# Kernel tuning notes

Hardware: AMD Instinct MI355X
Metric: run time of the kernel (lower is better)

Reference implementation:

```python
import jax, jax.numpy as jnp
import numpy as np

B, N, C = 2, 2048, 1024
H, D = 16, 64
EPS = 1e-12  # F.normalize eps


def l2norm(t):
    # torch F.normalize: t / max(||t||_2, eps)
    n = jnp.sqrt(jnp.sum(t * t, axis=-1, keepdims=True))
    return t / jnp.maximum(n, EPS)


def setup_inputs() -> dict:
    key = jax.random.key(0)
    ks = jax.random.split(key, 4)
    x = jax.random.normal(ks[0], (B, N, C), dtype=jnp.float32)
    W_qkv = jax.random.normal(ks[1], (C, 3 * H * D), dtype=jnp.float32) * (1.0 / np.sqrt(C))
    W_out = jax.random.normal(ks[2], (H * D, C), dtype=jnp.float32) * (1.0 / np.sqrt(H * D))
    pos_bias = jax.random.normal(ks[3], (H, N, N), dtype=jnp.float32) * 0.1
    temperature = jnp.array(15.5, dtype=jnp.float32)
    mask = jnp.zeros((B, N), dtype=bool)  # True = padded token
    return {"x": x, "W_qkv": W_qkv, "W_out": W_out, "temperature": temperature,
            "pos_bias": pos_bias, "mask": mask}


def reference(x, W_qkv, W_out, temperature, pos_bias, mask):
    b, n, c = x.shape
    # qkv projection; torch rearrange 'b n (h d qkv) -> qkv b h n d'
    qkv = (x @ W_qkv).reshape(b, n, H, D, 3)
    q = jnp.transpose(qkv[..., 0], (0, 2, 1, 3))  # b h n d
    k = jnp.transpose(qkv[..., 1], (0, 2, 1, 3))
    v = jnp.transpose(qkv[..., 2], (0, 2, 1, 3))
    q, k = l2norm(q), l2norm(k)
    dots = jnp.einsum('bhid,bhjd->bhij', q, k) * temperature
    dots = dots + pos_bias[None]  # broadcast over batch
    qkmask = ~mask  # True = valid
    allowed = qkmask[:, None, :, None] & qkmask[:, None, None, :]
    neg = -jnp.finfo(dots.dtype).max
    dots = jnp.where(allowed, dots, neg)
    attn = jax.nn.softmax(dots, axis=-1)
    out = jnp.einsum('bhij,bhjd->bhid', attn, v)
    out = jnp.transpose(out, (0, 2, 1, 3)).reshape(b, n, H * D)
    return out @ W_out
```

## Files before the change

kernel.cpp:

```cpp
#include <hip/hip_runtime.h>


using short4v = __attribute__((ext_vector_type(4))) short;
using short8 = __attribute__((ext_vector_type(8))) short;
using bf16x8 = __attribute__((ext_vector_type(8))) __bf16;
using f32x4  = __attribute__((ext_vector_type(4))) float;
using int4v  = __attribute__((ext_vector_type(4))) int;

constexpr int Bb = 2, Nn = 2048, Cc = 1024, Hh = 16, Dd = 64;

__device__ __forceinline__ unsigned short f2b(float f) {
  unsigned int u = __float_as_uint(f);
  u += 0x7FFFu + ((u >> 16) & 1u);
  return (unsigned short)(u >> 16);
}
__device__ __forceinline__ float b2f(unsigned short h) {
  return __uint_as_float(((unsigned int)h) << 16);
}
__device__ __forceinline__ f32x4 MFMA(short8 a, short8 b, f32x4 c) {
  return __builtin_amdgcn_mfma_f32_16x16x32_bf16(
      __builtin_bit_cast(bf16x8, a), __builtin_bit_cast(bf16x8, b), c, 0, 0, 0);
}
__device__ __forceinline__ unsigned cvtpk(float lo, float hi) {
  unsigned r;
  asm("v_cvt_pk_bf16_f32 %0, %1, %2" : "=v"(r) : "v"(lo), "v"(hi));
  return r;
}

__global__ void split_plain(const float* __restrict__ in, unsigned short* __restrict__ hi,
                            unsigned short* __restrict__ lo, int n) {
  int i = blockIdx.x * 256 + threadIdx.x;
  if (i < n) {
    float v = in[i];
    unsigned short t = f2b(v);
    hi[i] = t; lo[i] = f2b(v - b2f(t));
  }
}

__global__ __launch_bounds__(256) void split_trans2(
    const float* __restrict__ in, unsigned short* __restrict__ hi,
    unsigned short* __restrict__ lo, int K, int N) {
  __shared__ float t[32][33];
  int k0 = blockIdx.y * 32, n0 = blockIdx.x * 32;
  int tx = threadIdx.x & 31, ty = threadIdx.x >> 5;
  #pragma unroll
  for (int i = 0; i < 4; i++)
    t[ty + i * 8][tx] = in[(size_t)(k0 + ty + i * 8) * N + n0 + tx];
  __syncthreads();
  #pragma unroll
  for (int i = 0; i < 4; i++) {
    float v = t[tx][ty + i * 8];
    size_t o = (size_t)(n0 + ty + i * 8) * K + k0 + tx;
    unsigned short h = f2b(v);
    hi[o] = h; lo[o] = f2b(v - b2f(h));
  }
}

__global__ __launch_bounds__(256, 3) void gemm3(
    const unsigned short* __restrict__ Ah, const unsigned short* __restrict__ Al,
    const unsigned short* __restrict__ Bh, const unsigned short* __restrict__ Bl,
    float* __restrict__ C, int M, int N, int K) {
  __shared__ unsigned short sAh[128][40], sAl[128][40], sBh[128][40], sBl[128][40];
  int tid = threadIdx.x;
  int w = tid >> 6, l = tid & 63;
  int wr = w >> 1, wc = w & 1;
  int mrow = l & 15, kg = l >> 4;
  int row0 = blockIdx.y * 128, col0 = blockIdx.x * 128;
  f32x4 z = {0.f, 0.f, 0.f, 0.f};
  f32x4 acc[4][4];
  for (int i = 0; i < 4; i++) for (int j = 0; j < 4; j++) acc[i][j] = z;
  int sr = tid >> 1, sc0 = (tid & 1) * 16;
  for (int k0 = 0; k0 < K; k0 += 32) {
    const unsigned short* pa = Ah + (size_t)(row0 + sr) * K + k0 + sc0;
    const unsigned short* pal = Al + (size_t)(row0 + sr) * K + k0 + sc0;
    const unsigned short* pb = Bh + (size_t)(col0 + sr) * K + k0 + sc0;
    const unsigned short* pbl = Bl + (size_t)(col0 + sr) * K + k0 + sc0;
    short8 tA0 = *(const short8*)pa,  tA1 = *(const short8*)(pa + 8);
    short8 tL0 = *(const short8*)pal, tL1 = *(const short8*)(pal + 8);
    short8 tB0 = *(const short8*)pb,  tB1 = *(const short8*)(pb + 8);
    short8 tC0 = *(const short8*)pbl, tC1 = *(const short8*)(pbl + 8);
    __syncthreads();
    *(short8*)&sAh[sr][sc0] = tA0; *(short8*)&sAh[sr][sc0 + 8] = tA1;
    *(short8*)&sAl[sr][sc0] = tL0; *(short8*)&sAl[sr][sc0 + 8] = tL1;
    *(short8*)&sBh[sr][sc0] = tB0; *(short8*)&sBh[sr][sc0 + 8] = tB1;
    *(short8*)&sBl[sr][sc0] = tC0; *(short8*)&sBl[sr][sc0 + 8] = tC1;
    __syncthreads();
    short8 ah_[4], al_[4], bh_[4], bl_[4];
    #pragma unroll
    for (int mt = 0; mt < 4; mt++) {
      ah_[mt] = *(const short8*)&sAh[wr * 64 + mt * 16 + mrow][kg * 8];
      al_[mt] = *(const short8*)&sAl[wr * 64 + mt * 16 + mrow][kg * 8];
    }
    #pragma unroll
    for (int nt = 0; nt < 4; nt++) {
      bh_[nt] = *(const short8*)&sBh[wc * 64 + nt * 16 + mrow][kg * 8];
      bl_[nt] = *(const short8*)&sBl[wc * 64 + nt * 16 + mrow][kg * 8];
    }
    __builtin_amdgcn_s_setprio(1);
    #pragma unroll
    for (int mt = 0; mt < 4; mt++)
      #pragma unroll
      for (int nt = 0; nt < 4; nt++) {
        acc[mt][nt] = MFMA(ah_[mt], bh_[nt], acc[mt][nt]);
        acc[mt][nt] = MFMA(al_[mt], bh_[nt], acc[mt][nt]);
        acc[mt][nt] = MFMA(ah_[mt], bl_[nt], acc[mt][nt]);
      }
    __builtin_amdgcn_s_setprio(0);
  }
  #pragma unroll
  for (int mt = 0; mt < 4; mt++)
    #pragma unroll
    for (int nt = 0; nt < 4; nt++)
      #pragma unroll
      for (int q = 0; q < 4; q++) {
        int row = row0 + wr * 64 + mt * 16 + kg * 4 + q;
        int col = col0 + wc * 64 + nt * 16 + mrow;
        C[(size_t)row * N + col] = acc[mt][nt][q];
      }
}

__global__ __launch_bounds__(256) void qkv_post2(
    const float* __restrict__ qkv,
    unsigned short* __restrict__ qh, unsigned short* __restrict__ ql,
    unsigned short* __restrict__ kh, unsigned short* __restrict__ kl,
    unsigned short* __restrict__ vth) {
  __shared__ unsigned short vt[64][72];
  int tid = threadIdx.x, w = tid >> 6, d = tid & 63;
  int bid = blockIdx.x;
  int nb = bid & 31, h = (bid >> 5) & 15, b = bid >> 9;
  size_t head = (size_t)(b * Hh + h);
  int n0 = nb * 64;
  for (int it = 0; it < 16; it++) {
    int nl = w * 16 + it;
    int n = n0 + nl;
    const float* src = qkv + (size_t)(b * Nn + n) * 3072 + h * 192 + d * 3;
    float qv = src[0], kv = src[1], vv = src[2];
    float q2 = qv * qv, k2 = kv * kv;
    #pragma unroll
    for (int m = 1; m < 64; m <<= 1) { q2 += __shfl_xor(q2, m); k2 += __shfl_xor(k2, m); }
    qv /= fmaxf(sqrtf(q2), 1e-12f);
    kv /= fmaxf(sqrtf(k2), 1e-12f);
    size_t o = (head * Nn + n) * Dd + d;
    unsigned short tq = f2b(qv); qh[o] = tq; ql[o] = f2b(qv - b2f(tq));
    unsigned short tk = f2b(kv); kh[o] = tk; kl[o] = f2b(kv - b2f(tk));
    vt[nl][d] = f2b(vv);
  }
  __syncthreads();
  int r = tid >> 2, cq = (tid & 3) * 16;
  short8 x0, x1;
  #pragma unroll
  for (int i = 0; i < 8; i++) ((short*)&x0)[i] = (short)vt[cq + i][r];
  #pragma unroll
  for (int i = 0; i < 8; i++) ((short*)&x1)[i] = (short)vt[cq + 8 + i][r];
  unsigned short* dst = vth + (head * Dd + r) * Nn + n0 + cq;
  *(short8*)dst = x0;
  *(short8*)(dst + 8) = x1;
}

__global__ __launch_bounds__(256, 2) void flash_attn5(
    const unsigned short* __restrict__ qh_g, const unsigned short* __restrict__ ql_g,
    const unsigned short* __restrict__ kh_g, const unsigned short* __restrict__ kl_g,
    const unsigned short* __restrict__ vh_g,
    const float* __restrict__ bias, const float* __restrict__ tptr,
    unsigned short* __restrict__ ah, unsigned short* __restrict__ al) {
  __shared__ unsigned short sKh[2][64][64], sKl[2][64][64], sVh[2][64][64];
  int tid = threadIdx.x, w = tid >> 6, l = tid & 63;
  int mrow = l & 15, kg = l >> 4;
  int bid = blockIdx.x;
  int b = bid & 1, h = (bid >> 1) & 15, ib = bid >> 5;
  float T = tptr[0];
  const float L2E = 1.44269504f;
  float Tl2 = T * L2E;
  float negMs = -(T + 1.0f) * L2E;
  size_t head = (size_t)(b * Hh + h);
  int i0 = ib * 128 + w * 32;
  short8 aqh0[2], aql0[2], aqh1[2], aql1[2];
  {
    size_t qb0 = (head * Nn + i0 + mrow) * Dd;
    size_t qb1 = (head * Nn + i0 + 16 + mrow) * Dd;
    #pragma unroll
    for (int kk = 0; kk < 2; kk++) {
      aqh0[kk] = *(const short8*)(qh_g + qb0 + kk * 32 + kg * 8);
      aql0[kk] = *(const short8*)(ql_g + qb0 + kk * 32 + kg * 8);
      aqh1[kk] = *(const short8*)(qh_g + qb1 + kk * 32 + kg * 8);
      aql1[kk] = *(const short8*)(ql_g + qb1 + kk * 32 + kg * 8);
    }
  }
  f32x4 Ot0[4], Ot1[4];
  #pragma unroll
  for (int dt = 0; dt < 4; dt++) { Ot0[dt] = {0.f,0.f,0.f,0.f}; Ot1[dt] = {0.f,0.f,0.f,0.f}; }
  float L0 = 0.f, L1 = 0.f;

  int r0 = tid >> 3, c0 = (tid & 7) * 8;
  int r1 = r0 + 32;
  int lk0 = r0 * 64 + (c0 ^ ((r0 & 7) << 3));
  int lk1 = r1 * 64 + (c0 ^ ((r1 & 7) << 3));
  int pr0 = (r0 & 32) | ((r0 & 12) << 1) | ((r0 & 16) >> 2) | (r0 & 3);
  int pr1 = (r1 & 32) | ((r1 & 12) << 1) | ((r1 & 16) >> 2) | (r1 & 3);
  const unsigned short* kh_b = kh_g + head * Nn * Dd;
  const unsigned short* kl_b = kl_g + head * Nn * Dd;
  const unsigned short* vh_b = vh_g + head * Dd * Nn;
  const float* bbA = bias + ((size_t)h * Nn + i0 + mrow) * Nn + kg * 8;
  const float* bbB = bbA + (size_t)16 * Nn;

  short8 rKh0, rKh1, rKl0, rKl1, rVh0, rVh1;
  f32x4 rB0[4], rB1[4];

  auto issueKV = [&](int j0) {
    rKh0 = *(const short8*)(kh_b + (size_t)(j0 + pr0) * Dd + c0);
    rKh1 = *(const short8*)(kh_b + (size_t)(j0 + pr1) * Dd + c0);
    rKl0 = *(const short8*)(kl_b + (size_t)(j0 + pr0) * Dd + c0);
    rKl1 = *(const short8*)(kl_b + (size_t)(j0 + pr1) * Dd + c0);
    rVh0 = *(const short8*)(vh_b + (size_t)r0 * Nn + j0 + c0);
    rVh1 = *(const short8*)(vh_b + (size_t)r1 * Nn + j0 + c0);
  };
  auto writeKV = [&](int dst) {
    *(short8*)((unsigned short*)sKh[dst] + lk0) = rKh0;
    *(short8*)((unsigned short*)sKh[dst] + lk1) = rKh1;
    *(short8*)((unsigned short*)sKl[dst] + lk0) = rKl0;
    *(short8*)((unsigned short*)sKl[dst] + lk1) = rKl1;
    *(short8*)((unsigned short*)sVh[dst] + lk0) = rVh0;
    *(short8*)((unsigned short*)sVh[dst] + lk1) = rVh1;
  };
  auto issueBias = [&](int j0) {
    rB0[0] = *(const f32x4*)(bbA + j0);
    rB0[1] = *(const f32x4*)(bbA + j0 + 4);
    rB0[2] = *(const f32x4*)(bbA + j0 + 32);
    rB0[3] = *(const f32x4*)(bbA + j0 + 36);
    rB1[0] = *(const f32x4*)(bbB + j0);
    rB1[1] = *(const f32x4*)(bbB + j0 + 4);
    rB1[2] = *(const f32x4*)(bbB + j0 + 32);
    rB1[3] = *(const f32x4*)(bbB + j0 + 36);
    #pragma unroll
    for (int i = 0; i < 4; i++) {
      rB0[i] = rB0[i] * L2E + negMs;
      rB1[i] = rB1[i] * L2E + negMs;
    }
  };
  auto softmax = [&](f32x4* s, f32x4* rB, float& L_, short8& pf0, short8& pf1) {
    float p_[4][4];
    float ps = 0.f;
    #pragma unroll
    for (int jt = 0; jt < 4; jt++)
      #pragma unroll
      for (int q = 0; q < 4; q++) {
        p_[jt][q] = __builtin_amdgcn_exp2f(fmaf(s[jt][q], Tl2, rB[jt][q]));
        ps += p_[jt][q];
      }
    L_ += ps;
    unsigned pk[8];
    #pragma unroll
    for (int jt = 0; jt < 4; jt++) {
      pk[2 * jt]     = cvtpk(p_[jt][0], p_[jt][1]);
      pk[2 * jt + 1] = cvtpk(p_[jt][2], p_[jt][3]);
    }
    int4v w0 = {(int)pk[0], (int)pk[1], (int)pk[2], (int)pk[3]};
    int4v w1 = {(int)pk[4], (int)pk[5], (int)pk[6], (int)pk[7]};
    pf0 = __builtin_bit_cast(short8, w0);
    pf1 = __builtin_bit_cast(short8, w1);
  };

  issueKV(0);
  issueBias(0);
  writeKV(0);
  __syncthreads();
  issueKV(64);

  for (int t = 0; t < 32; t++) {
    int j0 = t * 64;
    int cur = t & 1;
    f32x4 s0[4], s1[4];
    #pragma unroll
    for (int jt = 0; jt < 4; jt++) { s0[jt] = {0.f,0.f,0.f,0.f}; s1[jt] = {0.f,0.f,0.f,0.f}; }
    __builtin_amdgcn_s_setprio(1);
    #pragma unroll
    for (int jt = 0; jt < 4; jt++) {
      int row = jt * 16 + mrow;
      int swz = (row & 7) << 3;
      #pragma unroll
      for (int kk = 0; kk < 2; kk++) {
        short8 bh = *(const short8*)&sKh[cur][row][(kk * 32 + kg * 8) ^ swz];
        short8 bl = *(const short8*)&sKl[cur][row][(kk * 32 + kg * 8) ^ swz];
        s0[jt] = MFMA(bh, aqh0[kk], s0[jt]);
        s0[jt] = MFMA(bh, aql0[kk], s0[jt]);
        s0[jt] = MFMA(bl, aqh0[kk], s0[jt]);
        s1[jt] = MFMA(bh, aqh1[kk], s1[jt]);
        s1[jt] = MFMA(bh, aql1[kk], s1[jt]);
        s1[jt] = MFMA(bl, aqh1[kk], s1[jt]);
      }
    }
    __builtin_amdgcn_s_setprio(0);
    short8 pfA0, pfA1, pfB0, pfB1;
    softmax(s0, rB0, L0, pfA0, pfA1);
    softmax(s1, rB1, L1, pfB0, pfB1);
    if (t < 31) issueBias(j0 + 64);
    if (t < 31) writeKV(cur ^ 1);
    if (t < 30) issueKV(j0 + 128);
    __builtin_amdgcn_s_setprio(1);
    #pragma unroll
    for (int dt = 0; dt < 4; dt++) {
      int row = dt * 16 + mrow;
      int swz = (row & 7) << 3;
      short8 va0 = *(const short8*)&sVh[cur][row][(kg * 8) ^ swz];
      short8 va1 = *(const short8*)&sVh[cur][row][(32 + kg * 8) ^ swz];
      Ot0[dt] = MFMA(va0, pfA0, Ot0[dt]);
      Ot0[dt] = MFMA(va1, pfA1, Ot0[dt]);
      Ot1[dt] = MFMA(va0, pfB0, Ot1[dt]);
      Ot1[dt] = MFMA(va1, pfB1, Ot1[dt]);
    }
    __builtin_amdgcn_s_setprio(0);
    __syncthreads();
  }
  L0 += __shfl_xor(L0, 16); L0 += __shfl_xor(L0, 32);
  L1 += __shfl_xor(L1, 16); L1 += __shfl_xor(L1, 32);
  float inv0 = 1.f / L0, inv1 = 1.f / L1;
  size_t orow0 = ((size_t)(b * Nn + i0 + mrow)) * (Hh * Dd) + h * Dd + kg * 4;
  size_t orow1 = ((size_t)(b * Nn + i0 + 16 + mrow)) * (Hh * Dd) + h * Dd + kg * 4;
  #pragma unroll
  for (int dt = 0; dt < 4; dt++) {
    short4v hi4, lo4;
    #pragma unroll
    for (int r = 0; r < 4; r++) {
      float val = Ot0[dt][r] * inv0;
      unsigned short hv = f2b(val);
      hi4[r] = (short)hv;
      lo4[r] = (short)f2b(val - b2f(hv));
    }
    *(short4v*)(ah + orow0 + dt * 16) = hi4;
    *(short4v*)(al + orow0 + dt * 16) = lo4;
    #pragma unroll
    for (int r = 0; r < 4; r++) {
      float val = Ot1[dt][r] * inv1;
      unsigned short hv = f2b(val);
      hi4[r] = (short)hv;
      lo4[r] = (short)f2b(val - b2f(hv));
    }
    *(short4v*)(ah + orow1 + dt * 16) = hi4;
    *(short4v*)(al + orow1 + dt * 16) = lo4;
  }
}

extern "C" void kernel_launch(void* const* d_in, const int* in_sizes, int n_in,
                              void* d_out, int out_size, void* d_ws, size_t ws_size,
                              hipStream_t stream) {
  const float* x    = (const float*)d_in[0];
  const float* Wqkv = (const float*)d_in[1];
  const float* Wout = (const float*)d_in[2];
  const float* temp = (const float*)d_in[3];
  const float* bias = (const float*)d_in[4];
  float* out = (float*)d_out;

  char* ws = (char*)d_ws;
  size_t off = 0;
  auto alloc = [&](size_t bytes) -> void* {
    void* p = ws + off;
    off += (bytes + 255) & ~(size_t)255;
    return p;
  };
  const size_t MT = (size_t)Bb * Nn;
  float* qkv = (float*)alloc(MT * 3072 * 4);
  unsigned short* xh  = (unsigned short*)alloc(MT * Cc * 2);
  unsigned short* xl  = (unsigned short*)alloc(MT * Cc * 2);
  unsigned short* wqh = (unsigned short*)alloc((size_t)3072 * Cc * 2);
  unsigned short* wql = (unsigned short*)alloc((size_t)3072 * Cc * 2);
  unsigned short* woh = (unsigned short*)alloc((size_t)Cc * Cc * 2);
  unsigned short* wol = (unsigned short*)alloc((size_t)Cc * Cc * 2);
  const size_t HND = (size_t)Bb * Hh * Nn * Dd;
  unsigned short* qh  = (unsigned short*)alloc(HND * 2);
  unsigned short* ql  = (unsigned short*)alloc(HND * 2);
  unsigned short* kh  = (unsigned short*)alloc(HND * 2);
  unsigned short* kl  = (unsigned short*)alloc(HND * 2);
  unsigned short* vth = (unsigned short*)alloc(HND * 2);
  unsigned short* ah  = (unsigned short*)alloc(MT * Cc * 2);
  unsigned short* al  = (unsigned short*)alloc(MT * Cc * 2);
  (void)ws_size; (void)in_sizes; (void)n_in; (void)out_size;

  split_plain<<<dim3((int)(MT * Cc / 256)), dim3(256), 0, stream>>>(x, xh, xl, (int)(MT * Cc));
  split_trans2<<<dim3(3072 / 32, Cc / 32), dim3(256), 0, stream>>>(Wqkv, wqh, wql, Cc, 3072);
  split_trans2<<<dim3(Cc / 32, Cc / 32), dim3(256), 0, stream>>>(Wout, woh, wol, Cc, Cc);

  gemm3<<<dim3(3072 / 128, (int)(MT / 128)), dim3(256), 0, stream>>>(
      xh, xl, wqh, wql, qkv, (int)MT, 3072, Cc);

  qkv_post2<<<dim3(Bb * Hh * (Nn / 64)), dim3(256), 0, stream>>>(
      qkv, qh, ql, kh, kl, vth);

  flash_attn5<<<dim3(Bb * Hh * (Nn / 128)), dim3(256), 0, stream>>>(
      qh, ql, kh, kl, vth, bias, temp, ah, al);

  gemm3<<<dim3(Cc / 128, (int)(MT / 128)), dim3(256), 0, stream>>>(
      ah, al, woh, wol, out, (int)MT, Cc, Cc);
}
```

Baseline: 294.5 us.

## Split attention KV range in two and merge partial results in a separate kernel

The flash attention kernel now handles only half of the key/value sequence per block, which doubles the grid. Each block writes unnormalized fp32 partial outputs and row sums into reused workspace. A new merge kernel adds the two partials, normalizes them, and produces the hi/lo bf16 split. The merge stays exact without a running-max correction because softmax uses a fixed upper-bound shift. The intent is more blocks and better load balance across CUs, at the cost of extra global traffic for the fp32 partials and one more kernel launch.

```diff
diff --git a/kernel.cpp b/kernel.cpp
--- a/kernel.cpp
+++ b/kernel.cpp
@@ -8,6 +8,7 @@
 using int4v  = __attribute__((ext_vector_type(4))) int;
 
 constexpr int Bb = 2, Nn = 2048, Cc = 1024, Hh = 16, Dd = 64;
+constexpr int SPLIT = 2, NSPL = Nn / SPLIT;
 
 __device__ __forceinline__ unsigned short f2b(float f) {
   unsigned int u = __float_as_uint(f);
@@ -157,17 +158,18 @@
   *(short8*)(dst + 8) = x1;
 }
 
-__global__ __launch_bounds__(256, 2) void flash_attn5(
+__global__ __launch_bounds__(256, 2) void flash_attn6(
     const unsigned short* __restrict__ qh_g, const unsigned short* __restrict__ ql_g,
     const unsigned short* __restrict__ kh_g, const unsigned short* __restrict__ kl_g,
     const unsigned short* __restrict__ vh_g,
     const float* __restrict__ bias, const float* __restrict__ tptr,
-    unsigned short* __restrict__ ah, unsigned short* __restrict__ al) {
+    float* __restrict__ Of, float* __restrict__ Lf) {
   __shared__ unsigned short sKh[2][64][64], sKl[2][64][64], sVh[2][64][64];
   int tid = threadIdx.x, w = tid >> 6, l = tid & 63;
   int mrow = l & 15, kg = l >> 4;
   int bid = blockIdx.x;
-  int b = bid & 1, h = (bid >> 1) & 15, ib = bid >> 5;
+  int s = bid & 1, ib = (bid >> 1) & 15, b = (bid >> 5) & 1, h = bid >> 6;
+  int jbase = s * NSPL;
   float T = tptr[0];
   const float L2E = 1.44269504f;
   float Tl2 = T * L2E;
@@ -237,14 +239,14 @@
       rB1[i] = rB1[i] * L2E + negMs;
     }
   };
-  auto softmax = [&](f32x4* s, f32x4* rB, float& L_, short8& pf0, short8& pf1) {
+  auto softmax = [&](f32x4* sx, f32x4* rB, float& L_, short8& pf0, short8& pf1) {
     float p_[4][4];
     float ps = 0.f;
     #pragma unroll
     for (int jt = 0; jt < 4; jt++)
       #pragma unroll
       for (int q = 0; q < 4; q++) {
-        p_[jt][q] = __builtin_amdgcn_exp2f(fmaf(s[jt][q], Tl2, rB[jt][q]));
+        p_[jt][q] = __builtin_amdgcn_exp2f(fmaf(sx[jt][q], Tl2, rB[jt][q]));
         ps += p_[jt][q];
       }
     L_ += ps;
@@ -260,14 +262,14 @@
     pf1 = __builtin_bit_cast(short8, w1);
   };
 
-  issueKV(0);
-  issueBias(0);
+  issueKV(jbase);
+  issueBias(jbase);
   writeKV(0);
   __syncthreads();
-  issueKV(64);
-
-  for (int t = 0; t < 32; t++) {
-    int j0 = t * 64;
+  issueKV(jbase + 64);
+
+  for (int t = 0; t < 16; t++) {
+    int j0 = jbase + t * 64;
     int cur = t & 1;
     f32x4 s0[4], s1[4];
     #pragma unroll
@@ -293,9 +295,9 @@
     short8 pfA0, pfA1, pfB0, pfB1;
     softmax(s0, rB0, L0, pfA0, pfA1);
     softmax(s1, rB1, L1, pfB0, pfB1);
-    if (t < 31) issueBias(j0 + 64);
-    if (t < 31) writeKV(cur ^ 1);
-    if (t < 30) issueKV(j0 + 128);
+    if (t < 15) issueBias(j0 + 64);
+    if (t < 15) writeKV(cur ^ 1);
+    if (t < 14) issueKV(j0 + 128);
     __builtin_amdgcn_s_setprio(1);
     #pragma unroll
     for (int dt = 0; dt < 4; dt++) {
@@ -313,31 +315,45 @@
   }
   L0 += __shfl_xor(L0, 16); L0 += __shfl_xor(L0, 32);
   L1 += __shfl_xor(L1, 16); L1 += __shfl_xor(L1, 32);
-  float inv0 = 1.f / L0, inv1 = 1.f / L1;
-  size_t orow0 = ((size_t)(b * Nn + i0 + mrow)) * (Hh * Dd) + h * Dd + kg * 4;
-  size_t orow1 = ((size_t)(b * Nn + i0 + 16 + mrow)) * (Hh * Dd) + h * Dd + kg * 4;
+  size_t prow0 = ((((size_t)s * Bb + b) * Hh + h) * Nn + i0 + mrow) * Dd + kg * 4;
+  size_t prow1 = prow0 + (size_t)16 * Dd;
   #pragma unroll
   for (int dt = 0; dt < 4; dt++) {
-    short4v hi4, lo4;
-    #pragma unroll
-    for (int r = 0; r < 4; r++) {
-      float val = Ot0[dt][r] * inv0;
-      unsigned short hv = f2b(val);
-      hi4[r] = (short)hv;
-      lo4[r] = (short)f2b(val - b2f(hv));
-    }
-    *(short4v*)(ah + orow0 + dt * 16) = hi4;
-    *(short4v*)(al + orow0 + dt * 16) = lo4;
-    #pragma unroll
-    for (int r = 0; r < 4; r++) {
-      float val = Ot1[dt][r] * inv1;
-      unsigned short hv = f2b(val);
-      hi4[r] = (short)hv;
-      lo4[r] = (short)f2b(val - b2f(hv));
-    }
-    *(short4v*)(ah + orow1 + dt * 16) = hi4;
-    *(short4v*)(al + orow1 + dt * 16) = lo4;
-  }
+    *(f32x4*)(Of + prow0 + dt * 16) = Ot0[dt];
+    *(f32x4*)(Of + prow1 + dt * 16) = Ot1[dt];
+  }
+  if (kg == 0) {
+    size_t lrow = (((size_t)s * Bb + b) * Hh + h) * Nn + i0 + mrow;
+    Lf[lrow] = L0;
+    Lf[lrow + 16] = L1;
+  }
+}
+
+__global__ __launch_bounds__(256) void attn_merge(
+    const float* __restrict__ Of, const float* __restrict__ Lf,
+    unsigned short* __restrict__ ah, unsigned short* __restrict__ al) {
+  int gid = blockIdx.x * 256 + threadIdx.x;
+  int row = gid >> 4;
+  int dq = (gid & 15) << 2;
+  int b = row >> 15, h = (row >> 11) & 15, i = row & 2047;
+  const size_t PS = (size_t)Bb * Hh * Nn * Dd;
+  const size_t LS = (size_t)Bb * Hh * Nn;
+  size_t base = ((size_t)(b * Hh + h) * Nn + i) * Dd + dq;
+  f32x4 o0 = *(const f32x4*)(Of + base);
+  f32x4 o1 = *(const f32x4*)(Of + PS + base);
+  size_t lb = (size_t)(b * Hh + h) * Nn + i;
+  float inv = 1.f / (Lf[lb] + Lf[LS + lb]);
+  short4v hi4, lo4;
+  #pragma unroll
+  for (int r = 0; r < 4; r++) {
+    float val = (o0[r] + o1[r]) * inv;
+    unsigned short hv = f2b(val);
+    hi4[r] = (short)hv;
+    lo4[r] = (short)f2b(val - b2f(hv));
+  }
+  size_t o = ((size_t)(b * Nn + i)) * (Hh * Dd) + h * Dd + dq;
+  *(short4v*)(ah + o) = hi4;
+  *(short4v*)(al + o) = lo4;
 }
 
 extern "C" void kernel_launch(void* const* d_in, const int* in_sizes, int n_in,
@@ -373,6 +389,8 @@
   unsigned short* vth = (unsigned short*)alloc(HND * 2);
   unsigned short* ah  = (unsigned short*)alloc(MT * Cc * 2);
   unsigned short* al  = (unsigned short*)alloc(MT * Cc * 2);
+  float* Of = qkv;
+  float* Lf = (float*)wqh;
   (void)ws_size; (void)in_sizes; (void)n_in; (void)out_size;
 
   split_plain<<<dim3((int)(MT * Cc / 256)), dim3(256), 0, stream>>>(x, xh, xl, (int)(MT * Cc));
@@ -385,8 +403,11 @@
   qkv_post2<<<dim3(Bb * Hh * (Nn / 64)), dim3(256), 0, stream>>>(
       qkv, qh, ql, kh, kl, vth);
 
-  flash_attn5<<<dim3(Bb * Hh * (Nn / 128)), dim3(256), 0, stream>>>(
-      qh, ql, kh, kl, vth, bias, temp, ah, al);
+  flash_attn6<<<dim3(Bb * Hh * (Nn / 128) * SPLIT), dim3(256), 0, stream>>>(
+      qh, ql, kh, kl, vth, bias, temp, Of, Lf);
+
+  attn_merge<<<dim3((int)(Bb * Hh * Nn * (Dd / 4) / 256)), dim3(256), 0, stream>>>(
+      Of, Lf, ah, al);
 
   gemm3<<<dim3(Cc / 128, (int)(MT / 128)), dim3(256), 0, stream>>>(
       ah, al, woh, wol, out, (int)MT, Cc, Cc);
```

After: 294.5 us. Within noise of the previous version (+0.0%).

## Load K and V fragments directly from global memory, dropping LDS staging

Applied to the files above, without the earlier changes.

The flash attention kernel stops staging K-high, K-low and V tiles in double-buffered shared memory. Each wave now loads its MFMA operand fragments straight from global memory (through L2 and L1) every iteration, and the per-iteration block barrier is removed. This cuts LDS traffic, shared-memory footprint and synchronisation. In exchange, the four waves in a block each fetch the same K/V data separately, so global and cache traffic rises, and there is no explicit prefetch to hide load latency.

```diff
diff --git a/kernel.cpp b/kernel.cpp
--- a/kernel.cpp
+++ b/kernel.cpp
@@ -157,13 +157,12 @@
   *(short8*)(dst + 8) = x1;
 }
 
-__global__ __launch_bounds__(256, 2) void flash_attn5(
+__global__ __launch_bounds__(256, 2) void flash_attn7(
     const unsigned short* __restrict__ qh_g, const unsigned short* __restrict__ ql_g,
     const unsigned short* __restrict__ kh_g, const unsigned short* __restrict__ kl_g,
     const unsigned short* __restrict__ vh_g,
     const float* __restrict__ bias, const float* __restrict__ tptr,
     unsigned short* __restrict__ ah, unsigned short* __restrict__ al) {
-  __shared__ unsigned short sKh[2][64][64], sKl[2][64][64], sVh[2][64][64];
   int tid = threadIdx.x, w = tid >> 6, l = tid & 63;
   int mrow = l & 15, kg = l >> 4;
   int bid = blockIdx.x;
@@ -191,37 +190,25 @@
   for (int dt = 0; dt < 4; dt++) { Ot0[dt] = {0.f,0.f,0.f,0.f}; Ot1[dt] = {0.f,0.f,0.f,0.f}; }
   float L0 = 0.f, L1 = 0.f;
 
-  int r0 = tid >> 3, c0 = (tid & 7) * 8;
-  int r1 = r0 + 32;
-  int lk0 = r0 * 64 + (c0 ^ ((r0 & 7) << 3));
-  int lk1 = r1 * 64 + (c0 ^ ((r1 & 7) << 3));
-  int pr0 = (r0 & 32) | ((r0 & 12) << 1) | ((r0 & 16) >> 2) | (r0 & 3);
-  int pr1 = (r1 & 32) | ((r1 & 12) << 1) | ((r1 & 16) >> 2) | (r1 & 3);
+  const unsigned short* kAh[4];
+  const unsigned short* kAl[4];
   const unsigned short* kh_b = kh_g + head * Nn * Dd;
   const unsigned short* kl_b = kl_g + head * Nn * Dd;
+  #pragma unroll
+  for (int jt = 0; jt < 4; jt++) {
+    int prow = ((jt & 2) << 4) | ((mrow & 12) << 1) | ((jt & 1) << 2) | (mrow & 3);
+    kAh[jt] = kh_b + (size_t)prow * Dd + kg * 8;
+    kAl[jt] = kl_b + (size_t)prow * Dd + kg * 8;
+  }
+  const unsigned short* vA[4];
   const unsigned short* vh_b = vh_g + head * Dd * Nn;
+  #pragma unroll
+  for (int dt = 0; dt < 4; dt++)
+    vA[dt] = vh_b + (size_t)(dt * 16 + mrow) * Nn + kg * 8;
   const float* bbA = bias + ((size_t)h * Nn + i0 + mrow) * Nn + kg * 8;
   const float* bbB = bbA + (size_t)16 * Nn;
 
-  short8 rKh0, rKh1, rKl0, rKl1, rVh0, rVh1;
   f32x4 rB0[4], rB1[4];
-
-  auto issueKV = [&](int j0) {
-    rKh0 = *(const short8*)(kh_b + (size_t)(j0 + pr0) * Dd + c0);
-    rKh1 = *(const short8*)(kh_b + (size_t)(j0 + pr1) * Dd + c0);
-    rKl0 = *(const short8*)(kl_b + (size_t)(j0 + pr0) * Dd + c0);
-    rKl1 = *(const short8*)(kl_b + (size_t)(j0 + pr1) * Dd + c0);
-    rVh0 = *(const short8*)(vh_b + (size_t)r0 * Nn + j0 + c0);
-    rVh1 = *(const short8*)(vh_b + (size_t)r1 * Nn + j0 + c0);
-  };
-  auto writeKV = [&](int dst) {
-    *(short8*)((unsigned short*)sKh[dst] + lk0) = rKh0;
-    *(short8*)((unsigned short*)sKh[dst] + lk1) = rKh1;
-    *(short8*)((unsigned short*)sKl[dst] + lk0) = rKl0;
-    *(short8*)((unsigned short*)sKl[dst] + lk1) = rKl1;
-    *(short8*)((unsigned short*)sVh[dst] + lk0) = rVh0;
-    *(short8*)((unsigned short*)sVh[dst] + lk1) = rVh1;
-  };
   auto issueBias = [&](int j0) {
     rB0[0] = *(const f32x4*)(bbA + j0);
     rB0[1] = *(const f32x4*)(bbA + j0 + 4);
@@ -237,14 +224,14 @@
       rB1[i] = rB1[i] * L2E + negMs;
     }
   };
-  auto softmax = [&](f32x4* s, f32x4* rB, float& L_, short8& pf0, short8& pf1) {
+  auto softmax = [&](f32x4* sx, f32x4* rB, float& L_, short8& pf0, short8& pf1) {
     float p_[4][4];
     float ps = 0.f;
     #pragma unroll
     for (int jt = 0; jt < 4; jt++)
       #pragma unroll
       for (int q = 0; q < 4; q++) {
-        p_[jt][q] = __builtin_amdgcn_exp2f(fmaf(s[jt][q], Tl2, rB[jt][q]));
+        p_[jt][q] = __builtin_amdgcn_exp2f(fmaf(sx[jt][q], Tl2, rB[jt][q]));
         ps += p_[jt][q];
       }
     L_ += ps;
@@ -260,56 +247,53 @@
     pf1 = __builtin_bit_cast(short8, w1);
   };
 
-  issueKV(0);
   issueBias(0);
-  writeKV(0);
-  __syncthreads();
-  issueKV(64);
 
   for (int t = 0; t < 32; t++) {
     int j0 = t * 64;
-    int cur = t & 1;
+    short8 bh_[4][2], bl_[4][2];
+    #pragma unroll
+    for (int jt = 0; jt < 4; jt++)
+      #pragma unroll
+      for (int kk = 0; kk < 2; kk++) {
+        bh_[jt][kk] = *(const short8*)(kAh[jt] + (size_t)j0 * Dd + kk * 32);
+        bl_[jt][kk] = *(const short8*)(kAl[jt] + (size_t)j0 * Dd + kk * 32);
+      }
     f32x4 s0[4], s1[4];
     #pragma unroll
     for (int jt = 0; jt < 4; jt++) { s0[jt] = {0.f,0.f,0.f,0.f}; s1[jt] = {0.f,0.f,0.f,0.f}; }
     __builtin_amdgcn_s_setprio(1);
     #pragma unroll
-    for (int jt = 0; jt < 4; jt++) {
-      int row = jt * 16 + mrow;
-      int swz = (row & 7) << 3;
+    for (int jt = 0; jt < 4; jt++)
       #pragma unroll
       for (int kk = 0; kk < 2; kk++) {
-        short8 bh = *(const short8*)&sKh[cur][row][(kk * 32 + kg * 8) ^ swz];
-        short8 bl = *(const short8*)&sKl[cur][row][(kk * 32 + kg * 8) ^ swz];
-        s0[jt] = MFMA(bh, aqh0[kk], s0[jt]);
-        s0[jt] = MFMA(bh, aql0[kk], s0[jt]);
-        s0[jt] = MFMA(bl, aqh0[kk], s0[jt]);
-        s1[jt] = MFMA(bh, aqh1[kk], s1[jt]);
-        s1[jt] = MFMA(bh, aql1[kk], s1[jt]);
-        s1[jt] = MFMA(bl, aqh1[kk], s1[jt]);
-      }
-    }
+        s0[jt] = MFMA(bh_[jt][kk], aqh0[kk], s0[jt]);
+        s0[jt] = MFMA(bh_[jt][kk], aql0[kk], s0[jt]);
+        s0[jt] = MFMA(bl_[jt][kk], aqh0[kk], s0[jt]);
+        s1[jt] = MFMA(bh_[jt][kk], aqh1[kk], s1[jt]);
+        s1[jt] = MFMA(bh_[jt][kk], aql1[kk], s1[jt]);
+        s1[jt] = MFMA(bl_[jt][kk], aqh1[kk], s1[jt]);
+      }
     __builtin_amdgcn_s_setprio(0);
+    short8 va_[4][2];
+    #pragma unroll
+    for (int dt = 0; dt < 4; dt++)
+      #pragma unroll
+      for (int k2 = 0; k2 < 2; k2++)
+        va_[dt][k2] = *(const short8*)(vA[dt] + j0 + k2 * 32);
     short8 pfA0, pfA1, pfB0, pfB1;
     softmax(s0, rB0, L0, pfA0, pfA1);
     softmax(s1, rB1, L1, pfB0, pfB1);
     if (t < 31) issueBias(j0 + 64);
-    if (t < 31) writeKV(cur ^ 1);
-    if (t < 30) issueKV(j0 + 128);
     __builtin_amdgcn_s_setprio(1);
     #pragma unroll
     for (int dt = 0; dt < 4; dt++) {
-      int row = dt * 16 + mrow;
-      int swz = (row & 7) << 3;
-      short8 va0 = *(const short8*)&sVh[cur][row][(kg * 8) ^ swz];
-      short8 va1 = *(const short8*)&sVh[cur][row][(32 + kg * 8) ^ swz];
-      Ot0[dt] = MFMA(va0, pfA0, Ot0[dt]);
-      Ot0[dt] = MFMA(va1, pfA1, Ot0[dt]);
-      Ot1[dt] = MFMA(va0, pfB0, Ot1[dt]);
-      Ot1[dt] = MFMA(va1, pfB1, Ot1[dt]);
+      Ot0[dt] = MFMA(va_[dt][0], pfA0, Ot0[dt]);
+      Ot0[dt] = MFMA(va_[dt][1], pfA1, Ot0[dt]);
+      Ot1[dt] = MFMA(va_[dt][0], pfB0, Ot1[dt]);
+      Ot1[dt] = MFMA(va_[dt][1], pfB1, Ot1[dt]);
     }
     __builtin_amdgcn_s_setprio(0);
-    __syncthreads();
   }
   L0 += __shfl_xor(L0, 16); L0 += __shfl_xor(L0, 32);
   L1 += __shfl_xor(L1, 16); L1 += __shfl_xor(L1, 32);
@@ -385,7 +369,7 @@
   qkv_post2<<<dim3(Bb * Hh * (Nn / 64)), dim3(256), 0, stream>>>(
       qkv, qh, ql, kh, kl, vth);
 
-  flash_attn5<<<dim3(Bb * Hh * (Nn / 128)), dim3(256), 0, stream>>>(
+  flash_attn7<<<dim3(Bb * Hh * (Nn / 128)), dim3(256), 0, stream>>>(
       qh, ql, kh, kl, vth, bias, temp, ah, al);
 
   gemm3<<<dim3(Cc / 128, (int)(MT / 128)), dim3(256), 0, stream>>>(
```

Result: slower. 407.8 us (+38.5%).
